# Performance work log

Measured on AMD Instinct MI355X. Metric: run time of the kernel, lower is better.

The kernel has to match this reference:

```python
import jax, jax.numpy as jnp
import numpy as np

T, B, C, L = 2000, 64, 256, 200  # frames, batch, vocab, target length
NEG_INF = jnp.float32(-1e30)


def setup_inputs() -> dict:
    key = jax.random.key(0)
    k1, k2 = jax.random.split(key)
    inputs = jax.random.normal(k1, (T, B, C), dtype=jnp.float32)
    targets = jax.random.randint(k2, (B, L), 0, C, dtype=jnp.int64)
    return {"inputs": inputs, "targets": targets}


def _transducer_loss(inputs, targets):
    # log-normalize emissions, then batch-major: [B, T, C]
    log_probs = jax.nn.log_softmax(inputs, axis=2)
    log_probs = jnp.transpose(log_probs, (1, 0, 2))
    Bn, Tn, Cn = log_probs.shape
    Ln = targets.shape[1]
    # emission score of target token l at frame t: emit[b, t, l]
    idx = jnp.broadcast_to(targets[:, None, :], (Bn, Tn, Ln))
    emit = jnp.take_along_axis(log_probs, idx, axis=2)  # [B, T, L]

    # Monotonic-alignment forward DP (gtn forward_score over the
    # composed emissions/alignment graph): at each frame either stay on the
    # current target token or advance to the next one; every token emitted >=1 frame.
    # alpha[b, l] = logsumexp over alignments of frames 0..t ending at token l.
    alpha0 = jnp.full((Bn, Ln), NEG_INF, dtype=log_probs.dtype).at[:, 0].set(emit[:, 0, 0])

    def step(alpha, e_t):
        shifted = jnp.concatenate(
            [jnp.full((Bn, 1), NEG_INF, dtype=alpha.dtype), alpha[:, :-1]], axis=1
        )
        alpha = e_t + jnp.logaddexp(alpha, shifted)
        return alpha, None

    emit_t_major = jnp.swapaxes(emit, 0, 1)  # [T, B, L]
    alpha, _ = jax.lax.scan(step, alpha0, emit_t_major[1:])

    # negative log-likelihood (scale = -1), averaged over the batch
    return jnp.mean(-alpha[:, -1])


def reference(inputs, targets):
    return _transducer_loss(inputs, targets)
```

## Files before the change

kernel.cpp:

```cpp
#include <hip/hip_runtime.h>

#define T_FRAMES 2000
#define BATCH    64
#define CVOC     256
#define LTGT     200
#define EPAD     200
#define SEG      20
#define NSEG     100
#define NEG_INF  (-1e30f)
#define INV_LN2  1.4426950408889634f
#define LN2      0.6931471805599453f
#define SCALE_LOG2 14.0f
#define DESCALE    (1.0f / 16384.0f)

#if __has_builtin(__builtin_amdgcn_exp2f)
__device__ __forceinline__ float fexp2(float x) { return __builtin_amdgcn_exp2f(x); }
#else
__device__ __forceinline__ float fexp2(float x) { return exp2f(x); }
#endif
#if __has_builtin(__builtin_amdgcn_logf)
__device__ __forceinline__ float flog2(float x) { return __builtin_amdgcn_logf(x); }
#else
__device__ __forceinline__ float flog2(float x) { return log2f(x); }
#endif

struct __align__(8) H4 { _Float16 x, y, z, w; };

__device__ __forceinline__ float dpp_shr1_zero(float v) {
    return __int_as_float(__builtin_amdgcn_update_dpp(
        0, __float_as_int(v), 0x138, 0xF, 0xF, true));
}
__device__ __forceinline__ int dpp_shr1_zero_i(int v) {
    return __builtin_amdgcn_update_dpp(0, v, 0x138, 0xF, 0xF, true);
}
template <int CTRL, int RMASK>
__device__ __forceinline__ float dpp_term(float v) {
    return __int_as_float(__builtin_amdgcn_update_dpp(
        0, __float_as_int(v), CTRL, RMASK, 0xF, true));
}
__device__ __forceinline__ float wave_max(float v) {
    v = fmaxf(v, dpp_term<0x111, 0xF>(v));
    v = fmaxf(v, dpp_term<0x112, 0xF>(v));
    v = fmaxf(v, dpp_term<0x114, 0xF>(v));
    v = fmaxf(v, dpp_term<0x118, 0xF>(v));
    v = fmaxf(v, dpp_term<0x142, 0xA>(v));
    v = fmaxf(v, dpp_term<0x143, 0xC>(v));
    return __int_as_float(__builtin_amdgcn_readlane(__float_as_int(v), 63));
}
__device__ __forceinline__ float wave_sum(float v) {
    v += dpp_term<0x111, 0xF>(v);
    v += dpp_term<0x112, 0xF>(v);
    v += dpp_term<0x114, 0xF>(v);
    v += dpp_term<0x118, 0xF>(v);
    v += dpp_term<0x142, 0xA>(v);
    v += dpp_term<0x143, 0xC>(v);
    return __int_as_float(__builtin_amdgcn_readlane(__float_as_int(v), 63));
}

__global__ __launch_bounds__(256) void emit_kernel(const float* __restrict__ x,
                                                   const int* __restrict__ targets,
                                                   _Float16* __restrict__ emit) {
    __shared__ float s[16][CVOC];
    const int w = threadIdx.x >> 6;
    const int lane = threadIdx.x & 63;
    const int r0 = blockIdx.x * 16 + w * 4;
    const int li = (lane < 50) ? lane : 49;

    float4 v[4];
#pragma unroll
    for (int k = 0; k < 4; ++k)
        v[k] = ((const float4*)(x + (size_t)(r0 + k) * CVOC))[lane];
    int4 tg[4];
#pragma unroll
    for (int k = 0; k < 4; ++k)
        tg[k] = ((const int4*)(targets + ((r0 + k) & 63) * LTGT))[li];

    float lse2[4];
#pragma unroll
    for (int k = 0; k < 4; ++k) {
        v[k].x *= INV_LN2; v[k].y *= INV_LN2; v[k].z *= INV_LN2; v[k].w *= INV_LN2;
        float m = fmaxf(fmaxf(v[k].x, v[k].y), fmaxf(v[k].z, v[k].w));
        m = wave_max(m);
        float ss = fexp2(v[k].x - m) + fexp2(v[k].y - m) +
                   fexp2(v[k].z - m) + fexp2(v[k].w - m);
        ss = wave_sum(ss);
        lse2[k] = m + flog2(ss);
        ((float4*)&s[w * 4 + k][lane * 4])[0] = v[k];
    }

#pragma unroll
    for (int k = 0; k < 4; ++k) {
        if (lane < 50) {
            const int r = r0 + k;
            const int t = r >> 6;
            const int b = r & 63;
            const float sc = SCALE_LOG2 - lse2[k];
            H4 h;
            h.x = (_Float16)fexp2(s[w * 4 + k][tg[k].x] + sc);
            h.y = (_Float16)fexp2(s[w * 4 + k][tg[k].y] + sc);
            h.z = (_Float16)fexp2(s[w * 4 + k][tg[k].z] + sc);
            h.w = (_Float16)fexp2(s[w * 4 + k][tg[k].w] + sc);
            ((H4*)(emit + ((size_t)b * T_FRAMES + t) * EPAD))[lane] = h;
        }
    }
}

__device__ __forceinline__ H4 ld_row(const _Float16* base, int t, int fi) {
    return ((const H4*)(base + (size_t)t * EPAD))[fi];
}

__device__ __forceinline__ void renorm(float& z0, float& z1, float& z2, float& z3,
                                       int& A) {
    const float m4 = fmaxf(fmaxf(z0, z1), fmaxf(z2, z3));
    const int Ap = dpp_shr1_zero_i(A);
    const bool act = (m4 > 0.0f);
    const int sh = act ? (127 - ((__float_as_int(m4) >> 23) & 255)) : 0;
    z0 = ldexpf(z0, sh); z1 = ldexpf(z1, sh);
    z2 = ldexpf(z2, sh); z3 = ldexpf(z3, sh);
    A = act ? (A - sh) : Ap;
}

__global__ __launch_bounds__(64, 1) void dp_kernel(const _Float16* __restrict__ emit,
                                                   float* __restrict__ part) {
    const int b = blockIdx.x;
    const int lane = threadIdx.x;
    const _Float16* base = emit + (size_t)b * T_FRAMES * EPAD;
    const int fi = (lane < 50) ? lane : 49;

    const float e00 = (float)base[0] * DESCALE;
    float z0 = (lane == 0) ? e00 : 0.0f;
    float z1 = 0.0f, z2 = 0.0f, z3 = 0.0f;
    int A = 0;
    renorm(z0, z1, z2, z3, A);

    float res = 1.0f;
    int resA = 0;

    H4 ebA[SEG], ebB[SEG];

#pragma unroll
    for (int j = 0; j < SEG; ++j)
        ebA[j] = ld_row(base, 1 + j, fi);

#define DP_STEP(e, tcur, j)                                           \
    {                                                                 \
        const float p  = dpp_shr1_zero(z3);                           \
        const int   Ap = dpp_shr1_zero_i(A);                          \
        const float pe = ldexpf(p, Ap - A);                           \
        const float e0 = (float)(e).x * DESCALE;                      \
        const float e1 = (float)(e).y * DESCALE;                      \
        const float e2 = (float)(e).z * DESCALE;                      \
        const float e3 = (float)(e).w * DESCALE;                      \
        const float n0 = e0 * (z0 + pe);                              \
        const float n1 = e1 * (z1 + z0);                              \
        const float n2 = e2 * (z2 + z1);                              \
        const float n3 = e3 * (z3 + z2);                              \
        z0 = n0; z1 = n1; z2 = n2; z3 = n3;                           \
        if ((tcur) == T_FRAMES - 1) { res = z3; resA = A; }           \
        if (((j) & 3) == 3) renorm(z0, z1, z2, z3, A);                \
    }

    for (int sp = 0; sp < NSEG; sp += 2) {
#pragma unroll
        for (int j = 0; j < SEG; ++j)
            ebB[j] = ld_row(base, 1 + (sp + 1) * SEG + j, fi);
#pragma unroll
        for (int j = 0; j < SEG; ++j)
            DP_STEP(ebA[j], 1 + sp * SEG + j, j);
        if (sp + 2 < NSEG) {
#pragma unroll
            for (int j = 0; j < SEG; ++j)
                ebA[j] = ld_row(base, 1 + (sp + 2) * SEG + j, fi);
        }
#pragma unroll
        for (int j = 0; j < SEG; ++j)
            DP_STEP(ebB[j], 1 + (sp + 1) * SEG + j, j);
    }
#undef DP_STEP

    const float rz = __int_as_float(__builtin_amdgcn_readlane(__float_as_int(res), 49));
    const int rA = __builtin_amdgcn_readlane(resA, 49);
    if (lane == 0) part[b] = -((float)rA + flog2(rz)) * LN2;
}

__global__ __launch_bounds__(64) void reduce_kernel(const float* __restrict__ part,
                                                    float* __restrict__ out) {
    float v = part[threadIdx.x];
#pragma unroll
    for (int s = 1; s < 64; s <<= 1) v += __shfl_xor(v, s, 64);
    if (threadIdx.x == 0) out[0] = v * (1.0f / BATCH);
}

__device__ __forceinline__ float lae(float a, float b) {
    float m = fmaxf(a, b);
    float d = fminf(a, b) - m;
    return m + __logf(1.0f + __expf(d));
}

__global__ __launch_bounds__(256) void lse_kernel(const float* __restrict__ x,
                                                  float* __restrict__ lse) {
    const int wave = threadIdx.x >> 6;
    const int lane = threadIdx.x & 63;
    const int r = blockIdx.x * 4 + wave;
    float4 v = ((const float4*)(x + (size_t)r * CVOC))[lane];
    float m = fmaxf(fmaxf(v.x, v.y), fmaxf(v.z, v.w));
#pragma unroll
    for (int s = 1; s < 64; s <<= 1) m = fmaxf(m, __shfl_xor(m, s, 64));
    float ssum = __expf(v.x - m) + __expf(v.y - m) + __expf(v.z - m) + __expf(v.w - m);
#pragma unroll
    for (int s = 1; s < 64; s <<= 1) ssum += __shfl_xor(ssum, s, 64);
    if (lane == 0) {
        const int t = r >> 6;
        const int b = r & 63;
        lse[b * T_FRAMES + t] = m + __logf(ssum);
    }
}

__global__ __launch_bounds__(64) void dp_slow_kernel(const float* __restrict__ x,
                                                     const int* __restrict__ targets,
                                                     const float* __restrict__ lse,
                                                     float* __restrict__ part) {
    __shared__ float s_lse[T_FRAMES];
    const int b = blockIdx.x;
    const int lane = threadIdx.x;
    for (int i = lane; i < T_FRAMES; i += 64) s_lse[i] = lse[b * T_FRAMES + i];
    const int* tg = targets + b * LTGT;
    const int l0 = lane * 4;
    const int i0 = tg[(l0 + 0 < LTGT) ? (l0 + 0) : (LTGT - 1)];
    const int i1 = tg[(l0 + 1 < LTGT) ? (l0 + 1) : (LTGT - 1)];
    const int i2 = tg[(l0 + 2 < LTGT) ? (l0 + 2) : (LTGT - 1)];
    const int i3 = tg[(l0 + 3 < LTGT) ? (l0 + 3) : (LTGT - 1)];
    const float* xb = x + b * CVOC;
    __syncthreads();
    float a0 = (lane == 0) ? (xb[i0] - s_lse[0]) : NEG_INF;
    float a1 = NEG_INF, a2 = NEG_INF, a3 = NEG_INF;
    const float* rA = xb + (size_t)1 * BATCH * CVOC;
    float pa0 = rA[i0], pa1 = rA[i1], pa2 = rA[i2], pa3 = rA[i3];
    const float* rB = xb + (size_t)2 * BATCH * CVOC;
    float pb0 = rB[i0], pb1 = rB[i1], pb2 = rB[i2], pb3 = rB[i3];
#define DP_STEP(e0, e1, e2, e3, tt)                                   \
    {                                                                 \
        const float ls = s_lse[tt];                                   \
        float prev = __shfl_up(a3, 1, 64);                            \
        if (lane == 0) prev = NEG_INF;                                \
        const float n0 = ((e0) - ls) + lae(a0, prev);                 \
        const float n1 = ((e1) - ls) + lae(a1, a0);                   \
        const float n2 = ((e2) - ls) + lae(a2, a1);                   \
        const float n3 = ((e3) - ls) + lae(a3, a2);                   \
        a0 = n0; a1 = n1; a2 = n2; a3 = n3;                           \
    }
    int t = 1;
    while (t < T_FRAMES) {
        DP_STEP(pa0, pa1, pa2, pa3, t);
        {
            const int tn = (t + 2 < T_FRAMES) ? (t + 2) : (T_FRAMES - 1);
            const float* r = xb + (size_t)tn * BATCH * CVOC;
            pa0 = r[i0]; pa1 = r[i1]; pa2 = r[i2]; pa3 = r[i3];
        }
        ++t;
        if (t >= T_FRAMES) break;
        DP_STEP(pb0, pb1, pb2, pb3, t);
        {
            const int tn = (t + 2 < T_FRAMES) ? (t + 2) : (T_FRAMES - 1);
            const float* r = xb + (size_t)tn * BATCH * CVOC;
            pb0 = r[i0]; pb1 = r[i1]; pb2 = r[i2]; pb3 = r[i3];
        }
        ++t;
    }
#undef DP_STEP
    const float resv = __shfl(a3, 49, 64);
    if (lane == 0) part[b] = -resv;
}

extern "C" void kernel_launch(void* const* d_in, const int* in_sizes, int n_in,
                              void* d_out, int out_size, void* d_ws, size_t ws_size,
                              hipStream_t stream) {
    const float* x = (const float*)d_in[0];
    const int* targets = (const int*)d_in[1];
    float* out = (float*)d_out;

    const size_t emit_bytes = (size_t)BATCH * T_FRAMES * EPAD * sizeof(_Float16);
    if (ws_size >= emit_bytes + 8192) {
        _Float16* emit = (_Float16*)d_ws;
        float* part = (float*)((char*)d_ws + emit_bytes + 4096);
        emit_kernel<<<T_FRAMES * BATCH / 16, 256, 0, stream>>>(x, targets, emit);
        dp_kernel<<<BATCH, 64, 0, stream>>>(emit, part);
        reduce_kernel<<<1, 64, 0, stream>>>(part, out);
    } else {
        float* lse = (float*)d_ws;
        float* part = lse + (size_t)BATCH * T_FRAMES;
        lse_kernel<<<T_FRAMES * BATCH / 4, 256, 0, stream>>>(x, lse);
        dp_slow_kernel<<<BATCH, 64, 0, stream>>>(x, targets, lse, part);
        reduce_kernel<<<1, 64, 0, stream>>>(part, out);
    }
}
```

Measured before the change: 281.7 us.

## Split alignment DP into concurrent forward and backward halves meeting at midpoint

The serial 2000-step forward DP becomes two chains run by separate blocks. One block runs forward over frames 1..999, the other runs backward from frame 1999 down to 1000, and a new combine kernel joins the two state vectors with a dot product and logsumexp. This halves the serial dependency length and uses 128 blocks instead of 64, at the cost of an extra kernel launch and extra workspace. It also drops the fp16 emission prescale of 2^14, which risks fp16 underflow or subnormals in stored emission probabilities.

```diff
diff --git a/kernel.cpp b/kernel.cpp
--- a/kernel.cpp
+++ b/kernel.cpp
@@ -6,12 +6,11 @@
 #define LTGT     200
 #define EPAD     200
 #define SEG      20
-#define NSEG     100
+#define NSEGH    50
+#define TSPLIT   999
 #define NEG_INF  (-1e30f)
 #define INV_LN2  1.4426950408889634f
 #define LN2      0.6931471805599453f
-#define SCALE_LOG2 14.0f
-#define DESCALE    (1.0f / 16384.0f)
 
 #if __has_builtin(__builtin_amdgcn_exp2f)
 __device__ __forceinline__ float fexp2(float x) { return __builtin_amdgcn_exp2f(x); }
@@ -33,6 +32,13 @@
 __device__ __forceinline__ int dpp_shr1_zero_i(int v) {
     return __builtin_amdgcn_update_dpp(0, v, 0x138, 0xF, 0xF, true);
 }
+__device__ __forceinline__ float dpp_shl1_zero(float v) {
+    return __int_as_float(__builtin_amdgcn_update_dpp(
+        0, __float_as_int(v), 0x130, 0xF, 0xF, true));
+}
+__device__ __forceinline__ int dpp_shl1_zero_i(int v) {
+    return __builtin_amdgcn_update_dpp(0, v, 0x130, 0xF, 0xF, true);
+}
 template <int CTRL, int RMASK>
 __device__ __forceinline__ float dpp_term(float v) {
     return __int_as_float(__builtin_amdgcn_update_dpp(
@@ -94,12 +100,11 @@
             const int r = r0 + k;
             const int t = r >> 6;
             const int b = r & 63;
-            const float sc = SCALE_LOG2 - lse2[k];
             H4 h;
-            h.x = (_Float16)fexp2(s[w * 4 + k][tg[k].x] + sc);
-            h.y = (_Float16)fexp2(s[w * 4 + k][tg[k].y] + sc);
-            h.z = (_Float16)fexp2(s[w * 4 + k][tg[k].z] + sc);
-            h.w = (_Float16)fexp2(s[w * 4 + k][tg[k].w] + sc);
+            h.x = (_Float16)fexp2(s[w * 4 + k][tg[k].x] - lse2[k]);
+            h.y = (_Float16)fexp2(s[w * 4 + k][tg[k].y] - lse2[k]);
+            h.z = (_Float16)fexp2(s[w * 4 + k][tg[k].z] - lse2[k]);
+            h.w = (_Float16)fexp2(s[w * 4 + k][tg[k].w] - lse2[k]);
             ((H4*)(emit + ((size_t)b * T_FRAMES + t) * EPAD))[lane] = h;
         }
     }
@@ -109,8 +114,8 @@
     return ((const H4*)(base + (size_t)t * EPAD))[fi];
 }
 
-__device__ __forceinline__ void renorm(float& z0, float& z1, float& z2, float& z3,
-                                       int& A) {
+__device__ __forceinline__ void renormF(float& z0, float& z1, float& z2, float& z3,
+                                        int& A) {
     const float m4 = fmaxf(fmaxf(z0, z1), fmaxf(z2, z3));
     const int Ap = dpp_shr1_zero_i(A);
     const bool act = (m4 > 0.0f);
@@ -119,68 +124,162 @@
     z2 = ldexpf(z2, sh); z3 = ldexpf(z3, sh);
     A = act ? (A - sh) : Ap;
 }
-
-__global__ __launch_bounds__(64, 1) void dp_kernel(const _Float16* __restrict__ emit,
-                                                   float* __restrict__ part) {
-    const int b = blockIdx.x;
+__device__ __forceinline__ void renormB(float& z0, float& z1, float& z2, float& z3,
+                                        int& A) {
+    const float m4 = fmaxf(fmaxf(z0, z1), fmaxf(z2, z3));
+    const int Ap = dpp_shl1_zero_i(A);
+    const bool act = (m4 > 0.0f);
+    const int sh = act ? (127 - ((__float_as_int(m4) >> 23) & 255)) : 0;
+    z0 = ldexpf(z0, sh); z1 = ldexpf(z1, sh);
+    z2 = ldexpf(z2, sh); z3 = ldexpf(z3, sh);
+    A = act ? (A - sh) : Ap;
+}
+
+__global__ __launch_bounds__(64, 1) void dp2_kernel(const _Float16* __restrict__ emit,
+                                                    float4* __restrict__ fz,
+                                                    int* __restrict__ fA,
+                                                    float4* __restrict__ bz,
+                                                    int* __restrict__ bA) {
+    const int bid = blockIdx.x;
+    const bool bwd = bid >= BATCH;
+    const int b = bwd ? (bid - BATCH) : bid;
     const int lane = threadIdx.x;
     const _Float16* base = emit + (size_t)b * T_FRAMES * EPAD;
     const int fi = (lane < 50) ? lane : 49;
 
-    const float e00 = (float)base[0] * DESCALE;
-    float z0 = (lane == 0) ? e00 : 0.0f;
-    float z1 = 0.0f, z2 = 0.0f, z3 = 0.0f;
-    int A = 0;
-    renorm(z0, z1, z2, z3, A);
-
-    float res = 1.0f;
-    int resA = 0;
-
     H4 ebA[SEG], ebB[SEG];
 
-#pragma unroll
-    for (int j = 0; j < SEG; ++j)
-        ebA[j] = ld_row(base, 1 + j, fi);
-
-#define DP_STEP(e, tcur, j)                                           \
+    if (!bwd) {
+        const float e00 = (float)base[0];
+        float z0 = (lane == 0) ? e00 : 0.0f;
+        float z1 = 0.0f, z2 = 0.0f, z3 = 0.0f;
+        int A = 0;
+        renormF(z0, z1, z2, z3, A);
+
+        float r0 = 0.0f, r1 = 0.0f, r2 = 0.0f, r3 = 0.0f;
+        int rA = 0;
+
+#pragma unroll
+        for (int j = 0; j < SEG; ++j)
+            ebA[j] = ld_row(base, 1 + j, fi);
+        __builtin_amdgcn_sched_barrier(0);
+
+#define DPF_STEP(e, tcur, j)                                          \
     {                                                                 \
         const float p  = dpp_shr1_zero(z3);                           \
         const int   Ap = dpp_shr1_zero_i(A);                          \
         const float pe = ldexpf(p, Ap - A);                           \
-        const float e0 = (float)(e).x * DESCALE;                      \
-        const float e1 = (float)(e).y * DESCALE;                      \
-        const float e2 = (float)(e).z * DESCALE;                      \
-        const float e3 = (float)(e).w * DESCALE;                      \
+        const float e0 = (float)(e).x;                                \
+        const float e1 = (float)(e).y;                                \
+        const float e2 = (float)(e).z;                                \
+        const float e3 = (float)(e).w;                                \
         const float n0 = e0 * (z0 + pe);                              \
         const float n1 = e1 * (z1 + z0);                              \
         const float n2 = e2 * (z2 + z1);                              \
         const float n3 = e3 * (z3 + z2);                              \
         z0 = n0; z1 = n1; z2 = n2; z3 = n3;                           \
-        if ((tcur) == T_FRAMES - 1) { res = z3; resA = A; }           \
-        if (((j) & 3) == 3) renorm(z0, z1, z2, z3, A);                \
-    }
-
-    for (int sp = 0; sp < NSEG; sp += 2) {
+        if ((tcur) == TSPLIT) { r0 = z0; r1 = z1; r2 = z2; r3 = z3; rA = A; } \
+        if (((j) & 3) == 3) renormF(z0, z1, z2, z3, A);               \
+    }
+
+        for (int sp = 0; sp < NSEGH; sp += 2) {
+#pragma unroll
+            for (int j = 0; j < SEG; ++j)
+                ebB[j] = ld_row(base, 1 + (sp + 1) * SEG + j, fi);
+            __builtin_amdgcn_sched_barrier(0);
+#pragma unroll
+            for (int j = 0; j < SEG; ++j)
+                DPF_STEP(ebA[j], 1 + sp * SEG + j, j);
+            __builtin_amdgcn_sched_barrier(0);
+            if (sp + 2 < NSEGH) {
+#pragma unroll
+                for (int j = 0; j < SEG; ++j)
+                    ebA[j] = ld_row(base, 1 + (sp + 2) * SEG + j, fi);
+                __builtin_amdgcn_sched_barrier(0);
+            }
+#pragma unroll
+            for (int j = 0; j < SEG; ++j)
+                DPF_STEP(ebB[j], 1 + (sp + 1) * SEG + j, j);
+            __builtin_amdgcn_sched_barrier(0);
+        }
+#undef DPF_STEP
+
+        fz[b * 64 + lane] = make_float4(r0, r1, r2, r3);
+        fA[b * 64 + lane] = rA;
+    } else {
+        float z0 = 0.0f, z1 = 0.0f, z2 = 0.0f;
+        float z3 = (lane == 49) ? 1.0f : 0.0f;
+        int A = 0;
+
 #pragma unroll
         for (int j = 0; j < SEG; ++j)
-            ebB[j] = ld_row(base, 1 + (sp + 1) * SEG + j, fi);
-#pragma unroll
-        for (int j = 0; j < SEG; ++j)
-            DP_STEP(ebA[j], 1 + sp * SEG + j, j);
-        if (sp + 2 < NSEG) {
-#pragma unroll
-            for (int j = 0; j < SEG; ++j)
-                ebA[j] = ld_row(base, 1 + (sp + 2) * SEG + j, fi);
+            ebA[j] = ld_row(base, 1999 - j, fi);
+        __builtin_amdgcn_sched_barrier(0);
+
+#define DPB_STEP(e, j)                                                \
+    {                                                                 \
+        const float e0 = (float)(e).x;                                \
+        const float e1 = (float)(e).y;                                \
+        const float e2 = (float)(e).z;                                \
+        const float e3 = (float)(e).w;                                \
+        const float w0 = z0 * e0;                                     \
+        const float w1 = z1 * e1;                                     \
+        const float w2 = z2 * e2;                                     \
+        const float w3 = z3 * e3;                                     \
+        const float q  = dpp_shl1_zero(w0);                           \
+        const int   Aq = dpp_shl1_zero_i(A);                          \
+        const float pe = ldexpf(q, Aq - A);                           \
+        z0 = w0 + w1; z1 = w1 + w2; z2 = w2 + w3; z3 = w3 + pe;       \
+        if (((j) & 3) == 3) renormB(z0, z1, z2, z3, A);               \
+    }
+
+        for (int sp = 0; sp < NSEGH; sp += 2) {
+#pragma unroll
+            for (int j = 0; j < SEG; ++j)
+                ebB[j] = ld_row(base, 1999 - ((sp + 1) * SEG + j), fi);
+            __builtin_amdgcn_sched_barrier(0);
+#pragma unroll
+            for (int j = 0; j < SEG; ++j)
+                DPB_STEP(ebA[j], j);
+            __builtin_amdgcn_sched_barrier(0);
+            if (sp + 2 < NSEGH) {
+#pragma unroll
+                for (int j = 0; j < SEG; ++j)
+                    ebA[j] = ld_row(base, 1999 - ((sp + 2) * SEG + j), fi);
+                __builtin_amdgcn_sched_barrier(0);
+            }
+#pragma unroll
+            for (int j = 0; j < SEG; ++j)
+                DPB_STEP(ebB[j], j);
+            __builtin_amdgcn_sched_barrier(0);
         }
-#pragma unroll
-        for (int j = 0; j < SEG; ++j)
-            DP_STEP(ebB[j], 1 + (sp + 1) * SEG + j, j);
-    }
-#undef DP_STEP
-
-    const float rz = __int_as_float(__builtin_amdgcn_readlane(__float_as_int(res), 49));
-    const int rA = __builtin_amdgcn_readlane(resA, 49);
-    if (lane == 0) part[b] = -((float)rA + flog2(rz)) * LN2;
+#undef DPB_STEP
+
+        bz[b * 64 + lane] = make_float4(z0, z1, z2, z3);
+        bA[b * 64 + lane] = A;
+    }
+}
+
+__global__ __launch_bounds__(64) void combine_kernel(const float4* __restrict__ fz,
+                                                     const int* __restrict__ fA,
+                                                     const float4* __restrict__ bz,
+                                                     const int* __restrict__ bA,
+                                                     float* __restrict__ part) {
+    const int b = blockIdx.x;
+    const int lane = threadIdx.x;
+    const float4 f = fz[b * 64 + lane];
+    const float4 g = bz[b * 64 + lane];
+    const float s = f.x * g.x + f.y * g.y + f.z * g.z + f.w * g.w;
+    float tl = (lane < 50 && s > 0.0f)
+                   ? flog2(s) + (float)(fA[b * 64 + lane] + bA[b * 64 + lane])
+                   : -3.0e38f;
+    float m = tl;
+#pragma unroll
+    for (int d = 1; d < 64; d <<= 1) m = fmaxf(m, __shfl_xor(m, d, 64));
+    float p = fexp2(tl - m);
+#pragma unroll
+    for (int d = 1; d < 64; d <<= 1) p += __shfl_xor(p, d, 64);
+    if (lane == 0) part[b] = -(m + flog2(p)) * LN2;
 }
 
 __global__ __launch_bounds__(64) void reduce_kernel(const float* __restrict__ part,
@@ -280,11 +379,23 @@
     float* out = (float*)d_out;
 
     const size_t emit_bytes = (size_t)BATCH * T_FRAMES * EPAD * sizeof(_Float16);
-    if (ws_size >= emit_bytes + 8192) {
+    const size_t off_part = emit_bytes + 4096;
+    const size_t off_fz   = emit_bytes + 8192;
+    const size_t off_fA   = off_fz + (size_t)BATCH * 64 * 16;
+    const size_t off_bz   = off_fA + (size_t)BATCH * 64 * 4;
+    const size_t off_bA   = off_bz + (size_t)BATCH * 64 * 16;
+    const size_t need     = off_bA + (size_t)BATCH * 64 * 4 + 4096;
+
+    if (ws_size >= need) {
         _Float16* emit = (_Float16*)d_ws;
-        float* part = (float*)((char*)d_ws + emit_bytes + 4096);
+        float*  part = (float*)((char*)d_ws + off_part);
+        float4* fz   = (float4*)((char*)d_ws + off_fz);
+        int*    fAi  = (int*)((char*)d_ws + off_fA);
+        float4* bz   = (float4*)((char*)d_ws + off_bz);
+        int*    bAi  = (int*)((char*)d_ws + off_bA);
         emit_kernel<<<T_FRAMES * BATCH / 16, 256, 0, stream>>>(x, targets, emit);
-        dp_kernel<<<BATCH, 64, 0, stream>>>(emit, part);
+        dp2_kernel<<<2 * BATCH, 64, 0, stream>>>(emit, fz, fAi, bz, bAi);
+        combine_kernel<<<BATCH, 64, 0, stream>>>(fz, fAi, bz, bAi, part);
         reduce_kernel<<<1, 64, 0, stream>>>(part, out);
     } else {
         float* lse = (float*)d_ws;
```

New measurement: 238.0 us. -15.5%, faster.
